# Kernel optimization log

Hardware: AMD Instinct MI355X
Metric: run time of the kernel (lower is better)

Reference implementation:

```python
import jax, jax.numpy as jnp
import numpy as np

EPS = 1e-8  # F.cosine_similarity default eps


def setup_inputs() -> dict:
    key = jax.random.key(0)
    k1, = jax.random.split(key, 1)
    x = jax.random.normal(k1, (16384, 512), dtype=jnp.float32)
    w = jnp.float32(10.0)   # init_w parameter
    b = jnp.float32(-5.0)   # init_b parameter
    return {"x": x, "w": w, "b": b}


def reference(x, w, b):
    # x: [2N, D] interleaved (anchor, positive) embeddings
    anchor = x[0::2]    # [N, D]
    positive = x[1::2]  # [N, D]
    N = anchor.shape[0]

    # cosine similarity matrix: cos[i, j] = <pos_i, anc_j> / max(|pos_i||anc_j|, eps)
    # (normalize + GEMM instead of the O(N*D*N) broadcast)
    dots = jnp.einsum('id,jd->ij', positive, anchor)          # [N, N]
    pn = jnp.linalg.norm(positive, axis=1)                    # [N]
    an = jnp.linalg.norm(anchor, axis=1)                      # [N]
    denom = jnp.maximum(pn[:, None] * an[None, :], EPS)
    cos_sim = dots / denom

    logits = cos_sim * w + b                                  # [N, N]
    labels = jnp.arange(N)

    # CrossEntropyLoss (mean reduction)
    logp = jax.nn.log_softmax(logits, axis=1)
    nloss = -jnp.mean(logp[jnp.arange(N), labels])
    return nloss
```

## Files before the change

### kernel.cpp

```cpp
#include <hip/hip_runtime.h>
#include <hip/hip_bf16.h>

typedef __attribute__((ext_vector_type(8))) short short8;
typedef __attribute__((ext_vector_type(4))) float f32x4;

#define D 512
#define BM 128
#define BN 128
#define BK 64

typedef const __attribute__((address_space(1))) void gvoid;
typedef __attribute__((address_space(3))) void lvoid;

__device__ inline unsigned pack2f(float lo, float hi) {
    __hip_bfloat162 v = __float22bfloat162_rn(make_float2(lo, hi));
    union { __hip_bfloat162 h; unsigned u; } cv;
    cv.h = v;
    return cv.u;
}

__device__ inline int4 pack8f(const float4& v0, const float4& v1, float sc) {
    int4 r;
    r.x = (int)pack2f(v0.x * sc, v0.y * sc);
    r.y = (int)pack2f(v0.z * sc, v0.w * sc);
    r.z = (int)pack2f(v1.x * sc, v1.y * sc);
    r.w = (int)pack2f(v1.z * sc, v1.w * sc);
    return r;
}

__global__ __launch_bounds__(256) void norm_kernel(
    const float* __restrict__ x,
    float* __restrict__ pinv, float* __restrict__ ainv,
    float* __restrict__ diag, float* __restrict__ sumexp,
    __hip_bfloat16* __restrict__ Pn, __hip_bfloat16* __restrict__ An, int cached)
{
    const int i = blockIdx.x, t = threadIdx.x;
    const float2* ap = (const float2*)(x + (size_t)(2 * i) * D);
    const float2* pp = (const float2*)(x + (size_t)(2 * i + 1) * D);
    float2 a = ap[t], p = pp[t];
    float ssa = a.x * a.x + a.y * a.y;
    float ssp = p.x * p.x + p.y * p.y;
    float dt  = p.x * a.x + p.y * a.y;
#pragma unroll
    for (int m = 1; m < 64; m <<= 1) {
        ssa += __shfl_xor(ssa, m);
        ssp += __shfl_xor(ssp, m);
        dt  += __shfl_xor(dt, m);
    }
    __shared__ float red[3][4];
    if ((t & 63) == 0) { int wv = t >> 6; red[0][wv] = ssa; red[1][wv] = ssp; red[2][wv] = dt; }
    __syncthreads();
    ssa = red[0][0] + red[0][1] + red[0][2] + red[0][3];
    ssp = red[1][0] + red[1][1] + red[1][2] + red[1][3];
    dt  = red[2][0] + red[2][1] + red[2][2] + red[2][3];
    float an = sqrtf(ssa), pn = sqrtf(ssp);
    float ia = 1.0f / fmaxf(an, 1e-30f);
    float ip = 1.0f / fmaxf(pn, 1e-30f);
    if (t == 0) {
        ainv[i] = ia;
        pinv[i] = ip;
        diag[i] = dt / fmaxf(pn * an, 1e-8f);
        sumexp[i] = 0.0f;
    }
    if (cached) {
        ((__hip_bfloat162*)(Pn + (size_t)i * D))[t] = __float22bfloat162_rn(make_float2(p.x * ip, p.y * ip));
        ((__hip_bfloat162*)(An + (size_t)i * D))[t] = __float22bfloat162_rn(make_float2(a.x * ia, a.y * ia));
    }
}

__global__ __launch_bounds__(256) void gemm_lse_128(
    const __hip_bfloat16* __restrict__ Pn, const __hip_bfloat16* __restrict__ An,
    const float* __restrict__ wp, float* __restrict__ sumexp)
{
    __shared__ __align__(16) unsigned char lds[32768];
    unsigned char* As = lds;
    unsigned char* Bs = lds + 16384;

    const int t = threadIdx.x;
    const int lane = t & 63, w = t >> 6;
    const int wr = w >> 1, wc = w & 1;
    const int l15 = lane & 15, lhi = lane >> 4;
    const int brow = blockIdx.y * BM;
    const int bcol = blockIdx.x * BN;

    const float wv = *wp;
    const float s = fabsf(wv);

    f32x4 acc[4][4];
#pragma unroll
    for (int mi = 0; mi < 4; ++mi)
#pragma unroll
        for (int ni = 0; ni < 4; ++ni)
#pragma unroll
            for (int j = 0; j < 4; ++j) acc[mi][ni][j] = 0.0f;

    const int o0 = t * 16;

    for (int kt = 0; kt < D / BK; ++kt) {
#pragma unroll
        for (int i = 0; i < 4; ++i) {
            int o = i * 4096 + o0;
            int row = o >> 7;
            int sslot = ((o >> 4) & 7) ^ (row & 7);
            const __hip_bfloat16* ga = Pn + (size_t)(brow + row) * D + kt * BK + sslot * 8;
            const __hip_bfloat16* gb = An + (size_t)(bcol + row) * D + kt * BK + sslot * 8;
            __builtin_amdgcn_global_load_lds((gvoid*)ga, (lvoid*)(As + o), 16, 0, 0);
            __builtin_amdgcn_global_load_lds((gvoid*)gb, (lvoid*)(Bs + o), 16, 0, 0);
        }
        __syncthreads();

#pragma unroll
        for (int ks = 0; ks < 2; ++ks) {
            short8 a[4], b[4];
            const int kb = ks * 64 + lhi * 16;
#pragma unroll
            for (int mi = 0; mi < 4; ++mi) {
                int r = wr * 64 + mi * 16 + l15;
                a[mi] = *(const short8*)(As + r * 128 + (kb ^ ((r & 7) << 4)));
            }
#pragma unroll
            for (int ni = 0; ni < 4; ++ni) {
                int c = wc * 64 + ni * 16 + l15;
                b[ni] = *(const short8*)(Bs + c * 128 + (kb ^ ((c & 7) << 4)));
            }
#pragma unroll
            for (int mi = 0; mi < 4; ++mi)
#pragma unroll
                for (int ni = 0; ni < 4; ++ni)
                    acc[mi][ni] = __builtin_amdgcn_mfma_f32_16x16x32_bf16(a[mi], b[ni], acc[mi][ni], 0, 0, 0);
        }
        __syncthreads();
    }

#pragma unroll
    for (int mi = 0; mi < 4; ++mi) {
#pragma unroll
        for (int j = 0; j < 4; ++j) {
            float v = 0.0f;
#pragma unroll
            for (int ni = 0; ni < 4; ++ni)
                v += __expf(acc[mi][ni][j] * wv - s);
            v += __shfl_xor(v, 1);
            v += __shfl_xor(v, 2);
            v += __shfl_xor(v, 4);
            v += __shfl_xor(v, 8);
            if (l15 == 0) {
                int row = brow + wr * 64 + mi * 16 + lhi * 4 + j;
                atomicAdd(&sumexp[row], v);
            }
        }
    }
}

__global__ __launch_bounds__(256, 2) void gemm_lse_small(
    const float* __restrict__ x,
    const float* __restrict__ pinv, const float* __restrict__ ainv,
    const float* __restrict__ wp, float* __restrict__ sumexp, int N)
{
    __shared__ __align__(16) unsigned char lds[81920];
    unsigned char* As = lds;
    unsigned char* Bs = lds + 65536;

    const int t = threadIdx.x;
    const int rb = blockIdx.y, cs = blockIdx.x;
    const int lane = t & 63, w = t >> 6;
    const int wr = w >> 1, wc = w & 1;
    const int l15 = lane & 15, lhi = lane >> 4;

    const int colsPer = N >> 3;
    const int CT = colsPer / 64;
    const int Q = CT * (D / 64);

    {
        int r = t >> 2;
        int kq = (t & 3) << 7;
        int grow = rb * 64 + r;
        const float4* src = (const float4*)(x + (size_t)(2 * grow + 1) * D);
        float sc = pinv[grow];
#pragma unroll
        for (int i2 = 0; i2 < 16; ++i2) {
            int k0 = kq + i2 * 8;
            float4 v0 = src[k0 >> 2], v1 = src[(k0 >> 2) + 1];
            *(int4*)(As + r * 1024 + ((k0 * 2) ^ ((r & 7) << 4))) = pack8f(v0, v1, sc);
        }
    }

    const int cl = t >> 2;
    const int kq = (t & 3) << 4;

    auto loadB = [&](int q, int4& oa, int4& ob) {
        int ct = q >> 3, kc = q & 7;
        int c = cs * colsPer + ct * 64 + cl;
        int k = kc * 64 + kq;
        const float4* src = (const float4*)(x + (size_t)(2 * c) * D + k);
        float sc = ainv[c];
        float4 v0 = src[0], v1 = src[1], v2 = src[2], v3 = src[3];
        oa = pack8f(v0, v1, sc);
        ob = pack8f(v2, v3, sc);
    };
    auto writeB = [&](int buf, const int4& oa, const int4& ob) {
        unsigned char* bb = Bs + buf * 8192 + cl * 128;
        int kb0 = kq * 2;
        *(int4*)(bb + (kb0 ^ ((cl & 7) << 4))) = oa;
        *(int4*)(bb + ((kb0 + 16) ^ ((cl & 7) << 4))) = ob;
    };

    const float wv = *wp;
    const float s = fabsf(wv);

    int4 ba, bb2;
    loadB(0, ba, bb2);
    __syncthreads();
    writeB(0, ba, bb2);
    __syncthreads();

    f32x4 acc[2][2];
    float rs[2][4];
#pragma unroll
    for (int mi = 0; mi < 2; ++mi) {
#pragma unroll
        for (int j = 0; j < 4; ++j) rs[mi][j] = 0.0f;
#pragma unroll
        for (int ni = 0; ni < 2; ++ni)
#pragma unroll
            for (int j = 0; j < 4; ++j) acc[mi][ni][j] = 0.0f;
    }

    for (int q = 0; q < Q; ++q) {
        const int kc = q & 7;
        const bool more = (q + 1 < Q);
        if (more) loadB(q + 1, ba, bb2);
        const unsigned char* Bp = Bs + (q & 1) * 8192;
#pragma unroll
        for (int ks = 0; ks < 2; ++ks) {
            int ka = kc * 64 + ks * 32 + lhi * 8;
            int ra0 = wr * 32 + l15, ra1 = ra0 + 16;
            short8 a0 = *(const short8*)(As + ra0 * 1024 + ((ka * 2) ^ ((ra0 & 7) << 4)));
            short8 a1 = *(const short8*)(As + ra1 * 1024 + ((ka * 2) ^ ((ra1 & 7) << 4)));
            int kb = ks * 32 + lhi * 8;
            int c0 = wc * 32 + l15, c1 = c0 + 16;
            short8 b0 = *(const short8*)(Bp + c0 * 128 + ((kb * 2) ^ ((c0 & 7) << 4)));
            short8 b1 = *(const short8*)(Bp + c1 * 128 + ((kb * 2) ^ ((c1 & 7) << 4)));
            acc[0][0] = __builtin_amdgcn_mfma_f32_16x16x32_bf16(a0, b0, acc[0][0], 0, 0, 0);
            acc[0][1] = __builtin_amdgcn_mfma_f32_16x16x32_bf16(a0, b1, acc[0][1], 0, 0, 0);
            acc[1][0] = __builtin_amdgcn_mfma_f32_16x16x32_bf16(a1, b0, acc[1][0], 0, 0, 0);
            acc[1][1] = __builtin_amdgcn_mfma_f32_16x16x32_bf16(a1, b1, acc[1][1], 0, 0, 0);
        }
        if (kc == 7) {
#pragma unroll
            for (int mi = 0; mi < 2; ++mi)
#pragma unroll
                for (int ni = 0; ni < 2; ++ni)
#pragma unroll
                    for (int j = 0; j < 4; ++j) {
                        rs[mi][j] += __expf(acc[mi][ni][j] * wv - s);
                        acc[mi][ni][j] = 0.0f;
                    }
        }
        if (more) {
            __syncthreads();
            writeB((q + 1) & 1, ba, bb2);
            __syncthreads();
        }
    }

#pragma unroll
    for (int mi = 0; mi < 2; ++mi)
#pragma unroll
        for (int j = 0; j < 4; ++j) {
            float v = rs[mi][j];
            v += __shfl_xor(v, 1);
            v += __shfl_xor(v, 2);
            v += __shfl_xor(v, 4);
            v += __shfl_xor(v, 8);
            if (l15 == 0) {
                int row = rb * 64 + wr * 32 + mi * 16 + lhi * 4 + j;
                atomicAdd(&sumexp[row], v);
            }
        }
}

__global__ __launch_bounds__(1024) void finalize_kernel(
    const float* __restrict__ sumexp, const float* __restrict__ diag,
    const float* __restrict__ wp, float* __restrict__ out, int N)
{
    const int t = threadIdx.x;
    const float w = *wp;
    const float s = fabsf(w);
    float acc = 0.0f;
    for (int i = t; i < N; i += 1024)
        acc += s + logf(sumexp[i]) - w * diag[i];
#pragma unroll
    for (int m = 1; m < 64; m <<= 1) acc += __shfl_xor(acc, m);
    __shared__ float red[16];
    if ((t & 63) == 0) red[t >> 6] = acc;
    __syncthreads();
    if (t == 0) {
        float v = 0.0f;
#pragma unroll
        for (int i = 0; i < 16; ++i) v += red[i];
        out[0] = v / (float)N;
    }
}

extern "C" void kernel_launch(void* const* d_in, const int* in_sizes, int n_in,
                              void* d_out, int out_size, void* d_ws, size_t ws_size,
                              hipStream_t stream) {
    const float* x  = (const float*)d_in[0];
    const float* wp = (const float*)d_in[1];

    const int N = in_sizes[0] / (2 * D);

    char* ws = (char*)d_ws;
    size_t nf = (size_t)N * 4;
    float* pinv   = (float*)(ws);
    float* ainv   = (float*)(ws + nf);
    float* diag   = (float*)(ws + 2 * nf);
    float* sumexp = (float*)(ws + 3 * nf);
    size_t base = (4 * nf + 255) & ~(size_t)255;
    __hip_bfloat16* Pn = (__hip_bfloat16*)(ws + base);
    __hip_bfloat16* An = (__hip_bfloat16*)(ws + base + (size_t)N * D * 2);
    const bool cached = ws_size >= base + (size_t)N * D * 4;

    norm_kernel<<<N, 256, 0, stream>>>(x, pinv, ainv, diag, sumexp, Pn, An, cached ? 1 : 0);

    if (cached) {
        dim3 grid(N / BN, N / BM);
        gemm_lse_128<<<grid, 256, 0, stream>>>(Pn, An, wp, sumexp);
    } else {
        dim3 grid(8, N / 64);
        gemm_lse_small<<<grid, 256, 0, stream>>>(x, pinv, ainv, wp, sumexp, N);
    }

    finalize_kernel<<<1, 1024, 0, stream>>>(sumexp, diag, wp, (float*)d_out, N);
}
```

Baseline: 237.1 us.

## Use 256x256 double-buffered GEMM tile with XCD remap and wave-per-row norm

The GEMM moves from a 128x128 single-buffered tile to a 256x256 tile with 8 waves. LDS is double-buffered so the next K-slice's global-to-LDS loads run while the current one is computed, and MFMA phases are interleaved with barriers and setprio. Workgroup IDs are remapped across the 8 XCDs to improve L2 locality. The norm kernel now has one wave per row pair using float4 loads, which drops the block-level LDS reduction. The cost is 128KB of LDS and higher register pressure, which may limit occupancy to 1 workgroup per CU despite the launch bound of 2.

```diff
diff --git a/kernel.cpp b/kernel.cpp
--- a/kernel.cpp
+++ b/kernel.cpp
@@ -5,9 +5,7 @@
 typedef __attribute__((ext_vector_type(4))) float f32x4;
 
 #define D 512
-#define BM 128
-#define BN 128
-#define BK 64
+#define NT 8
 
 typedef const __attribute__((address_space(1))) void gvoid;
 typedef __attribute__((address_space(3))) void lvoid;
@@ -28,112 +26,187 @@
     return r;
 }
 
-__global__ __launch_bounds__(256) void norm_kernel(
+__global__ __launch_bounds__(512) void norm_kernel(
     const float* __restrict__ x,
-    float* __restrict__ pinv, float* __restrict__ ainv,
     float* __restrict__ diag, float* __restrict__ sumexp,
-    __hip_bfloat16* __restrict__ Pn, __hip_bfloat16* __restrict__ An, int cached)
+    __hip_bfloat16* __restrict__ Pn, __hip_bfloat16* __restrict__ An)
 {
-    const int i = blockIdx.x, t = threadIdx.x;
-    const float2* ap = (const float2*)(x + (size_t)(2 * i) * D);
-    const float2* pp = (const float2*)(x + (size_t)(2 * i + 1) * D);
-    float2 a = ap[t], p = pp[t];
-    float ssa = a.x * a.x + a.y * a.y;
-    float ssp = p.x * p.x + p.y * p.y;
-    float dt  = p.x * a.x + p.y * a.y;
+    const int t = threadIdx.x;
+    const int i = blockIdx.x * 8 + (t >> 6);
+    const int lane = t & 63;
+    const float4* ap = (const float4*)(x + (size_t)(2 * i) * D);
+    const float4* pp = (const float4*)(x + (size_t)(2 * i + 1) * D);
+    float4 a0 = ap[lane * 2], a1 = ap[lane * 2 + 1];
+    float4 p0 = pp[lane * 2], p1 = pp[lane * 2 + 1];
+    float ssa = a0.x*a0.x + a0.y*a0.y + a0.z*a0.z + a0.w*a0.w
+              + a1.x*a1.x + a1.y*a1.y + a1.z*a1.z + a1.w*a1.w;
+    float ssp = p0.x*p0.x + p0.y*p0.y + p0.z*p0.z + p0.w*p0.w
+              + p1.x*p1.x + p1.y*p1.y + p1.z*p1.z + p1.w*p1.w;
+    float dt  = p0.x*a0.x + p0.y*a0.y + p0.z*a0.z + p0.w*a0.w
+              + p1.x*a1.x + p1.y*a1.y + p1.z*a1.z + p1.w*a1.w;
 #pragma unroll
     for (int m = 1; m < 64; m <<= 1) {
         ssa += __shfl_xor(ssa, m);
         ssp += __shfl_xor(ssp, m);
         dt  += __shfl_xor(dt, m);
     }
-    __shared__ float red[3][4];
-    if ((t & 63) == 0) { int wv = t >> 6; red[0][wv] = ssa; red[1][wv] = ssp; red[2][wv] = dt; }
-    __syncthreads();
-    ssa = red[0][0] + red[0][1] + red[0][2] + red[0][3];
-    ssp = red[1][0] + red[1][1] + red[1][2] + red[1][3];
-    dt  = red[2][0] + red[2][1] + red[2][2] + red[2][3];
     float an = sqrtf(ssa), pn = sqrtf(ssp);
     float ia = 1.0f / fmaxf(an, 1e-30f);
     float ip = 1.0f / fmaxf(pn, 1e-30f);
-    if (t == 0) {
-        ainv[i] = ia;
-        pinv[i] = ip;
+    if (lane == 0) {
         diag[i] = dt / fmaxf(pn * an, 1e-8f);
         sumexp[i] = 0.0f;
     }
-    if (cached) {
-        ((__hip_bfloat162*)(Pn + (size_t)i * D))[t] = __float22bfloat162_rn(make_float2(p.x * ip, p.y * ip));
-        ((__hip_bfloat162*)(An + (size_t)i * D))[t] = __float22bfloat162_rn(make_float2(a.x * ia, a.y * ia));
-    }
-}
-
-__global__ __launch_bounds__(256) void gemm_lse_128(
+    int4 wp_, wa_;
+    wp_ = pack8f(make_float4(p0.x,p0.y,p0.z,p0.w), make_float4(p1.x,p1.y,p1.z,p1.w), ip);
+    wa_ = pack8f(make_float4(a0.x,a0.y,a0.z,a0.w), make_float4(a1.x,a1.y,a1.z,a1.w), ia);
+    ((int4*)(Pn + (size_t)i * D))[lane] = wp_;
+    ((int4*)(An + (size_t)i * D))[lane] = wa_;
+}
+
+__global__ __launch_bounds__(512, 2) void gemm_lse_256(
     const __hip_bfloat16* __restrict__ Pn, const __hip_bfloat16* __restrict__ An,
-    const float* __restrict__ wp, float* __restrict__ sumexp)
+    const float* __restrict__ wp, float* __restrict__ sumexp, int nbx)
 {
-    __shared__ __align__(16) unsigned char lds[32768];
-    unsigned char* As = lds;
-    unsigned char* Bs = lds + 16384;
+    __shared__ __align__(16) unsigned char lds[131072];
 
     const int t = threadIdx.x;
     const int lane = t & 63, w = t >> 6;
-    const int wr = w >> 1, wc = w & 1;
+    const int wm = w >> 2, wn = w & 3;
     const int l15 = lane & 15, lhi = lane >> 4;
-    const int brow = blockIdx.y * BM;
-    const int bcol = blockIdx.x * BN;
+    const int swz = (l15 & 7) << 4;
+    const int kb0 = lhi * 16, kb1 = 64 + lhi * 16;
+
+    const int nwg = nbx * nbx;
+    const int cpx = nwg >> 3;
+    const int bid = blockIdx.x;
+    const int wgid = (bid & 7) * cpx + (bid >> 3);
+    const int brow = (wgid / nbx) * 256;
+    const int bcol = (wgid % nbx) * 256;
 
     const float wv = *wp;
     const float s = fabsf(wv);
 
-    f32x4 acc[4][4];
-#pragma unroll
-    for (int mi = 0; mi < 4; ++mi)
+    const int o_0 = t * 16, o_1 = t * 16 + 8192;
+    const int rl0 = o_0 >> 7, rl1 = o_1 >> 7;
+    const int ss0 = ((o_0 >> 4) & 7) ^ (rl0 & 7);
+    const int ss1 = ((o_1 >> 4) & 7) ^ (rl1 & 7);
+
+    const __hip_bfloat16* pa[2][2];
+    const __hip_bfloat16* pb[2][2];
+#pragma unroll
+    for (int hf = 0; hf < 2; ++hf) {
+        pa[hf][0] = Pn + (size_t)(brow + hf * 128 + rl0) * D + ss0 * 8;
+        pa[hf][1] = Pn + (size_t)(brow + hf * 128 + rl1) * D + ss1 * 8;
+        pb[hf][0] = An + (size_t)(bcol + hf * 128 + rl0) * D + ss0 * 8;
+        pb[hf][1] = An + (size_t)(bcol + hf * 128 + rl1) * D + ss1 * 8;
+    }
+
+    auto stage = [&](int dn) {
+        unsigned char* lA = lds + dn * 32768;
+        unsigned char* lB = lds + 65536 + dn * 32768;
+#pragma unroll
+        for (int hf = 0; hf < 2; ++hf) {
+            __builtin_amdgcn_global_load_lds((gvoid*)pa[hf][0], (lvoid*)(lA + hf * 16384 + o_0), 16, 0, 0);
+            __builtin_amdgcn_global_load_lds((gvoid*)pa[hf][1], (lvoid*)(lA + hf * 16384 + o_1), 16, 0, 0);
+            __builtin_amdgcn_global_load_lds((gvoid*)pb[hf][0], (lvoid*)(lB + hf * 16384 + o_0), 16, 0, 0);
+            __builtin_amdgcn_global_load_lds((gvoid*)pb[hf][1], (lvoid*)(lB + hf * 16384 + o_1), 16, 0, 0);
+            pa[hf][0] += 64; pa[hf][1] += 64;
+            pb[hf][0] += 64; pb[hf][1] += 64;
+        }
+    };
+
+    f32x4 acc[8][4];
+#pragma unroll
+    for (int mi = 0; mi < 8; ++mi)
 #pragma unroll
         for (int ni = 0; ni < 4; ++ni)
 #pragma unroll
             for (int j = 0; j < 4; ++j) acc[mi][ni][j] = 0.0f;
 
-    const int o0 = t * 16;
-
-    for (int kt = 0; kt < D / BK; ++kt) {
-#pragma unroll
-        for (int i = 0; i < 4; ++i) {
-            int o = i * 4096 + o0;
-            int row = o >> 7;
-            int sslot = ((o >> 4) & 7) ^ (row & 7);
-            const __hip_bfloat16* ga = Pn + (size_t)(brow + row) * D + kt * BK + sslot * 8;
-            const __hip_bfloat16* gb = An + (size_t)(bcol + row) * D + kt * BK + sslot * 8;
-            __builtin_amdgcn_global_load_lds((gvoid*)ga, (lvoid*)(As + o), 16, 0, 0);
-            __builtin_amdgcn_global_load_lds((gvoid*)gb, (lvoid*)(Bs + o), 16, 0, 0);
-        }
-        __syncthreads();
-
-#pragma unroll
-        for (int ks = 0; ks < 2; ++ks) {
-            short8 a[4], b[4];
-            const int kb = ks * 64 + lhi * 16;
-#pragma unroll
-            for (int mi = 0; mi < 4; ++mi) {
-                int r = wr * 64 + mi * 16 + l15;
-                a[mi] = *(const short8*)(As + r * 128 + (kb ^ ((r & 7) << 4)));
-            }
-#pragma unroll
-            for (int ni = 0; ni < 4; ++ni) {
-                int c = wc * 64 + ni * 16 + l15;
-                b[ni] = *(const short8*)(Bs + c * 128 + (kb ^ ((c & 7) << 4)));
-            }
+    stage(0);
+    asm volatile("s_waitcnt vmcnt(0)" ::: "memory");
+    __builtin_amdgcn_s_barrier();
+
+    short8 a[2][4], b0[2][2], b1[2][2];
+
+    for (int tn = 0; tn < NT; ++tn) {
+        const int c = tn & 1;
+        const unsigned char* lAc = lds + c * 32768 + wm * 16384 + l15 * 128;
+        const unsigned char* lBc = lds + 65536 + c * 32768 + (wn >> 1) * 16384 + ((wn & 1) * 64 + l15) * 128;
+
+#pragma unroll
+        for (int mi = 0; mi < 4; ++mi) {
+            a[0][mi] = *(const short8*)(lAc + mi * 2048 + (kb0 ^ swz));
+            a[1][mi] = *(const short8*)(lAc + mi * 2048 + (kb1 ^ swz));
+        }
+#pragma unroll
+        for (int nf = 0; nf < 2; ++nf) {
+            b0[0][nf] = *(const short8*)(lBc + nf * 2048 + (kb0 ^ swz));
+            b0[1][nf] = *(const short8*)(lBc + nf * 2048 + (kb1 ^ swz));
+        }
+        if (tn < NT - 1) stage(c ^ 1);
+        __builtin_amdgcn_s_barrier();
+        __builtin_amdgcn_s_setprio(1);
+#pragma unroll
+        for (int ks = 0; ks < 2; ++ks)
 #pragma unroll
             for (int mi = 0; mi < 4; ++mi)
 #pragma unroll
-                for (int ni = 0; ni < 4; ++ni)
-                    acc[mi][ni] = __builtin_amdgcn_mfma_f32_16x16x32_bf16(a[mi], b[ni], acc[mi][ni], 0, 0, 0);
-        }
-        __syncthreads();
-    }
-
-#pragma unroll
-    for (int mi = 0; mi < 4; ++mi) {
+                for (int nf = 0; nf < 2; ++nf)
+                    acc[mi][nf] = __builtin_amdgcn_mfma_f32_16x16x32_bf16(a[ks][mi], b0[ks][nf], acc[mi][nf], 0, 0, 0);
+        __builtin_amdgcn_s_setprio(0);
+        __builtin_amdgcn_s_barrier();
+
+#pragma unroll
+        for (int nf = 0; nf < 2; ++nf) {
+            b1[0][nf] = *(const short8*)(lBc + 4096 + nf * 2048 + (kb0 ^ swz));
+            b1[1][nf] = *(const short8*)(lBc + 4096 + nf * 2048 + (kb1 ^ swz));
+        }
+        __builtin_amdgcn_s_barrier();
+        __builtin_amdgcn_s_setprio(1);
+#pragma unroll
+        for (int ks = 0; ks < 2; ++ks)
+#pragma unroll
+            for (int mi = 0; mi < 4; ++mi)
+#pragma unroll
+                for (int nf = 0; nf < 2; ++nf)
+                    acc[mi][2 + nf] = __builtin_amdgcn_mfma_f32_16x16x32_bf16(a[ks][mi], b1[ks][nf], acc[mi][2 + nf], 0, 0, 0);
+        __builtin_amdgcn_s_setprio(0);
+        __builtin_amdgcn_s_barrier();
+
+#pragma unroll
+        for (int mi = 0; mi < 4; ++mi) {
+            a[0][mi] = *(const short8*)(lAc + 8192 + mi * 2048 + (kb0 ^ swz));
+            a[1][mi] = *(const short8*)(lAc + 8192 + mi * 2048 + (kb1 ^ swz));
+        }
+        __builtin_amdgcn_s_barrier();
+        __builtin_amdgcn_s_setprio(1);
+#pragma unroll
+        for (int ks = 0; ks < 2; ++ks)
+#pragma unroll
+            for (int mi = 0; mi < 4; ++mi)
+#pragma unroll
+                for (int nf = 0; nf < 2; ++nf)
+                    acc[4 + mi][2 + nf] = __builtin_amdgcn_mfma_f32_16x16x32_bf16(a[ks][mi], b1[ks][nf], acc[4 + mi][2 + nf], 0, 0, 0);
+        __builtin_amdgcn_s_setprio(0);
+        __builtin_amdgcn_s_barrier();
+
+        __builtin_amdgcn_s_setprio(1);
+#pragma unroll
+        for (int ks = 0; ks < 2; ++ks)
+#pragma unroll
+            for (int mi = 0; mi < 4; ++mi)
+#pragma unroll
+                for (int nf = 0; nf < 2; ++nf)
+                    acc[4 + mi][nf] = __builtin_amdgcn_mfma_f32_16x16x32_bf16(a[ks][mi], b0[ks][nf], acc[4 + mi][nf], 0, 0, 0);
+        __builtin_amdgcn_s_setprio(0);
+        asm volatile("s_waitcnt vmcnt(0) lgkmcnt(0)" ::: "memory");
+        __builtin_amdgcn_s_barrier();
+    }
+
+#pragma unroll
+    for (int mi = 0; mi < 8; ++mi) {
 #pragma unroll
         for (int j = 0; j < 4; ++j) {
             float v = 0.0f;
@@ -145,7 +218,7 @@
             v += __shfl_xor(v, 4);
             v += __shfl_xor(v, 8);
             if (l15 == 0) {
-                int row = brow + wr * 64 + mi * 16 + lhi * 4 + j;
+                int row = brow + wm * 128 + mi * 16 + lhi * 4 + j;
                 atomicAdd(&sumexp[row], v);
             }
         }
@@ -280,6 +353,39 @@
         }
 }
 
+__global__ __launch_bounds__(512) void norm_small(
+    const float* __restrict__ x,
+    float* __restrict__ pinv, float* __restrict__ ainv,
+    float* __restrict__ diag, float* __restrict__ sumexp)
+{
+    const int t = threadIdx.x;
+    const int i = blockIdx.x * 8 + (t >> 6);
+    const int lane = t & 63;
+    const float4* ap = (const float4*)(x + (size_t)(2 * i) * D);
+    const float4* pp = (const float4*)(x + (size_t)(2 * i + 1) * D);
+    float4 a0 = ap[lane * 2], a1 = ap[lane * 2 + 1];
+    float4 p0 = pp[lane * 2], p1 = pp[lane * 2 + 1];
+    float ssa = a0.x*a0.x + a0.y*a0.y + a0.z*a0.z + a0.w*a0.w
+              + a1.x*a1.x + a1.y*a1.y + a1.z*a1.z + a1.w*a1.w;
+    float ssp = p0.x*p0.x + p0.y*p0.y + p0.z*p0.z + p0.w*p0.w
+              + p1.x*p1.x + p1.y*p1.y + p1.z*p1.z + p1.w*p1.w;
+    float dt  = p0.x*a0.x + p0.y*a0.y + p0.z*a0.z + p0.w*a0.w
+              + p1.x*a1.x + p1.y*a1.y + p1.z*a1.z + p1.w*a1.w;
+#pragma unroll
+    for (int m = 1; m < 64; m <<= 1) {
+        ssa += __shfl_xor(ssa, m);
+        ssp += __shfl_xor(ssp, m);
+        dt  += __shfl_xor(dt, m);
+    }
+    float an = sqrtf(ssa), pn = sqrtf(ssp);
+    if (lane == 0) {
+        ainv[i] = 1.0f / fmaxf(an, 1e-30f);
+        pinv[i] = 1.0f / fmaxf(pn, 1e-30f);
+        diag[i] = dt / fmaxf(pn * an, 1e-8f);
+        sumexp[i] = 0.0f;
+    }
+}
+
 __global__ __launch_bounds__(1024) void finalize_kernel(
     const float* __restrict__ sumexp, const float* __restrict__ diag,
     const float* __restrict__ wp, float* __restrict__ out, int N)
@@ -322,12 +428,12 @@
     __hip_bfloat16* An = (__hip_bfloat16*)(ws + base + (size_t)N * D * 2);
     const bool cached = ws_size >= base + (size_t)N * D * 4;
 
-    norm_kernel<<<N, 256, 0, stream>>>(x, pinv, ainv, diag, sumexp, Pn, An, cached ? 1 : 0);
-
     if (cached) {
-        dim3 grid(N / BN, N / BM);
-        gemm_lse_128<<<grid, 256, 0, stream>>>(Pn, An, wp, sumexp);
+        norm_kernel<<<N / 8, 512, 0, stream>>>(x, diag, sumexp, Pn, An);
+        const int nbx = N / 256;
+        gemm_lse_256<<<nbx * nbx, 512, 0, stream>>>(Pn, An, wp, sumexp, nbx);
     } else {
+        norm_small<<<N / 8, 512, 0, stream>>>(x, pinv, ainv, diag, sumexp);
         dim3 grid(8, N / 64);
         gemm_lse_small<<<grid, 256, 0, stream>>>(x, pinv, ainv, wp, sumexp, N);
     }
```

New measurement: 223.7 us. -5.6%, faster.
